# Optimization experiments

Hardware: AMD Instinct MI355X
Metric: run time of the kernel (lower is better)

Reference implementation:

```python
import jax, jax.numpy as jnp
import numpy as np

N_INTT = 100000
N_MVTX = 100000
N_EDGES = 300000
IN_DIM = 64
OUT_DIM = 64
FEAT_DIM = 2 * OUT_DIM          # 128
EDGE_DIM = 2 * FEAT_DIM         # 256
H_DIM = IN_DIM + FEAT_DIM + 2 * EDGE_DIM  # 64+128+512 = 704


def _lin(key, fan_in, fan_out):
    k1, k2 = jax.random.split(key)
    bound = 1.0 / np.sqrt(fan_in)
    W = jax.random.uniform(k1, (fan_in, fan_out), jnp.float32, -bound, bound)
    b = jax.random.uniform(k2, (fan_out,), jnp.float32, -bound, bound)
    return W, b


def setup_inputs() -> dict:
    key = jax.random.key(0)
    ks = jax.random.split(key, 12)
    x_intt_0 = jax.random.normal(ks[0], (N_INTT, 3), jnp.float32)
    x_mvtx_0 = jax.random.normal(ks[1], (N_MVTX, 3), jnp.float32)
    x_intt = jax.random.normal(ks[2], (N_INTT, IN_DIM), jnp.float32)
    x_mvtx = jax.random.normal(ks[3], (N_MVTX, IN_DIM), jnp.float32)
    start = jax.random.randint(ks[4], (N_EDGES,), 0, N_INTT, jnp.int32)
    end = jax.random.randint(ks[5], (N_EDGES,), 0, N_MVTX, jnp.int32)
    edge_index = jnp.stack([start, end], axis=0)
    W_in_intt, b_in_intt = _lin(ks[6], IN_DIM, FEAT_DIM)
    W_in_mvtx, b_in_mvtx = _lin(ks[7], IN_DIM, FEAT_DIM)
    W_score, b_score = _lin(ks[8], EDGE_DIM, 1)
    W_out_intt, b_out_intt = _lin(ks[9], H_DIM, OUT_DIM)
    W_out_mvtx, b_out_mvtx = _lin(ks[10], H_DIM, OUT_DIM)
    return {
        "x_intt_0": x_intt_0, "x_mvtx_0": x_mvtx_0,
        "x_intt": x_intt, "x_mvtx": x_mvtx, "edge_index": edge_index,
        "W_in_intt": W_in_intt, "b_in_intt": b_in_intt,
        "W_in_mvtx": W_in_mvtx, "b_in_mvtx": b_in_mvtx,
        "W_score": W_score, "b_score": b_score,
        "W_out_intt": W_out_intt, "b_out_intt": b_out_intt,
        "W_out_mvtx": W_out_mvtx, "b_out_mvtx": b_out_mvtx,
    }


def _mean_max_pool(edges, idx, num_segments):
    # scatter_mean with zero-initialized out: mean over incident edges, 0 if none
    s = jax.ops.segment_sum(edges, idx, num_segments=num_segments)
    cnt = jax.ops.segment_sum(jnp.ones((edges.shape[0], 1), edges.dtype), idx,
                              num_segments=num_segments)
    mean = s / jnp.maximum(cnt, 1.0)
    # scatter_max with zero-initialized out: max includes the initial 0
    mx = jnp.maximum(jax.ops.segment_max(edges, idx, num_segments=num_segments), 0.0)
    return mean, mx


def reference(x_intt_0, x_mvtx_0, x_intt, x_mvtx, edge_index,
              W_in_intt, b_in_intt, W_in_mvtx, b_in_mvtx,
              W_score, b_score, W_out_intt, b_out_intt,
              W_out_mvtx, b_out_mvtx):
    # apply_constraints=False -> x_intt_0/x_mvtx_0 unused
    xp_intt = x_intt @ W_in_intt + b_in_intt        # [Ni, F]
    xp_mvtx = x_mvtx @ W_in_mvtx + b_in_mvtx        # [Nm, F]
    start, end = edge_index[0], edge_index[1]
    xp = jnp.concatenate([xp_intt[start], xp_mvtx[end]], axis=-1)  # [E, 2F]
    att = jnp.exp(-jnp.abs(xp @ W_score + b_score))  # potential activation, [E,1]
    edges = xp * att                                 # [E, 2F]
    mean_i, max_i = _mean_max_pool(edges, start, xp_intt.shape[0])
    mean_m, max_m = _mean_max_pool(edges, end, xp_mvtx.shape[0])
    H_intt = jnp.concatenate([x_intt, xp_intt, mean_i, max_i], axis=-1)  # [Ni, 704]
    H_mvtx = jnp.concatenate([x_mvtx, xp_mvtx, mean_m, max_m], axis=-1)
    h_intt = jax.nn.relu(H_intt @ W_out_intt + b_out_intt)
    h_mvtx = jax.nn.relu(H_mvtx @ W_out_mvtx + b_out_mvtx)
    return (h_intt, h_mvtx)
```

## Files before the change

### kernel.cpp

```cpp
#include <hip/hip_runtime.h>
#include <hip/hip_bf16.h>

typedef __hip_bfloat16 bf16;
typedef __attribute__((ext_vector_type(8))) short bf16x8;
typedef __attribute__((ext_vector_type(4))) float f32x4;

__device__ __forceinline__ float bfu(unsigned u) { return __uint_as_float(u << 16); }
__device__ __forceinline__ unsigned packbf(float a, float b) {
    return (unsigned)__bfloat16_as_ushort(__float2bfloat16(a)) |
           ((unsigned)__bfloat16_as_ushort(__float2bfloat16(b)) << 16);
}

#define CAP 32

#define NEL_O (704 * 64)
#define NEL_I (64 * 128)
__global__ __launch_bounds__(256) void setup_kernel(
    const int* __restrict__ e_start, const int* __restrict__ e_end,
    int* __restrict__ deg_i, int* __restrict__ deg_m,
    int* __restrict__ list_i, int* __restrict__ list_m, int E, int fill_blocks,
    const float* __restrict__ Woi, const float* __restrict__ Wom,
    bf16* __restrict__ Wtoi, bf16* __restrict__ Wtom,
    const float* __restrict__ Wii, const float* __restrict__ Wim,
    bf16* __restrict__ Wtii, bf16* __restrict__ Wtim)
{
    if ((int)blockIdx.x < fill_blocks) {
        int i = blockIdx.x * 256 + threadIdx.x;
        if (i >= E) return;
        int s = e_start[i], e = e_end[i];
        int pi = atomicAdd(&deg_i[s], 1);
        if (pi < CAP) list_i[(size_t)s * CAP + pi] = e;
        int pm = atomicAdd(&deg_m[e], 1);
        if (pm < CAP) list_m[(size_t)e * CAP + pm] = s;
        return;
    }
    int tid = (blockIdx.x - fill_blocks) * 256 + threadIdx.x;
    if (tid < 2 * NEL_O) {
        int half = tid >= NEL_O;
        int t = tid - half * NEL_O;
        int j = t / 704, k = t % 704;
        const float* W = half ? Wom : Woi;
        bf16* Wt = half ? Wtom : Wtoi;
        Wt[(size_t)j * 704 + k] = __float2bfloat16(W[(size_t)k * 64 + j]);
        return;
    }
    int t2 = tid - 2 * NEL_O;
    if (t2 >= 2 * NEL_I) return;
    int half = t2 >= NEL_I;
    int t = t2 - half * NEL_I;
    int c = t / 64, k = t % 64;
    const float* W = half ? Wim : Wii;
    bf16* Wt = half ? Wtim : Wtii;
    Wt[(size_t)c * 64 + k] = __float2bfloat16(W[(size_t)k * 128 + c]);
}

__global__ __launch_bounds__(256) void lin_in_mfma(
    const float* __restrict__ x_i, const bf16* __restrict__ Wt_ii,
    const float* __restrict__ b_i,
    const float* __restrict__ x_m, const bf16* __restrict__ Wt_im,
    const float* __restrict__ b_m,
    const float* __restrict__ Wsc,
    bf16* __restrict__ xp_i, bf16* __restrict__ xp_m,
    float* __restrict__ sc_i, float* __restrict__ sc_m,
    int Ni, int Nm, int blocks_i)
{
    int side = (int)blockIdx.x >= blocks_i;
    int blk = side ? blockIdx.x - blocks_i : blockIdx.x;
    const float* x  = side ? x_m : x_i;
    const bf16* Wt  = side ? Wt_im : Wt_ii;
    const float* b  = side ? b_m : b_i;
    const float* wsc = side ? Wsc + 128 : Wsc;
    bf16* xp = side ? xp_m : xp_i;
    float* sc = side ? sc_m : sc_i;
    int N = side ? Nm : Ni;

    int tid = threadIdx.x, wv = tid >> 6, lane = tid & 63;
    int frow = lane & 15, kg = lane >> 4;
    int n0 = blk * 64 + wv * 16;
    if (n0 >= N) return;
    int nrow = min(n0 + frow, N - 1);
    f32x4 acc[8];
#pragma unroll
    for (int nt = 0; nt < 8; ++nt) acc[nt] = (f32x4){0.f, 0.f, 0.f, 0.f};
#pragma unroll
    for (int kk = 0; kk < 2; ++kk) {
        const float* ap = x + (size_t)nrow * 64 + kk * 32 + kg * 8;
        float4 a0 = *(const float4*)ap;
        float4 a1 = *(const float4*)(ap + 4);
        union { unsigned u[4]; bf16x8 v; } au;
        au.u[0] = packbf(a0.x, a0.y); au.u[1] = packbf(a0.z, a0.w);
        au.u[2] = packbf(a1.x, a1.y); au.u[3] = packbf(a1.z, a1.w);
#pragma unroll
        for (int nt = 0; nt < 8; ++nt) {
            bf16x8 bf = *(const bf16x8*)(Wt + (size_t)(nt * 16 + frow) * 64 + kk * 32 + kg * 8);
            acc[nt] = __builtin_amdgcn_mfma_f32_16x16x32_bf16(au.v, bf, acc[nt], 0, 0, 0);
        }
    }
    float contrib[4] = {0.f, 0.f, 0.f, 0.f};
#pragma unroll
    for (int nt = 0; nt < 8; ++nt) {
        int col = nt * 16 + frow;
        float bj = b[col];
        float wj = wsc[col];
#pragma unroll
        for (int reg = 0; reg < 4; ++reg) {
            float v = acc[nt][reg] + bj;
            int n = n0 + kg * 4 + reg;
            if (n < N) xp[(size_t)n * 128 + col] = __float2bfloat16(v);
            contrib[reg] += v * wj;
        }
    }
#pragma unroll
    for (int off = 1; off < 16; off <<= 1) {
#pragma unroll
        for (int reg = 0; reg < 4; ++reg)
            contrib[reg] += __shfl_xor(contrib[reg], off, 64);
    }
    if (frow == 0) {
#pragma unroll
        for (int reg = 0; reg < 4; ++reg) {
            int n = n0 + kg * 4 + reg;
            if (n < N) sc[n] = contrib[reg];
        }
    }
}

#define BN 16
#define HS 712
__device__ __forceinline__ void accum8(uint4 g, float att, float* s, float* m) {
    unsigned gg[4] = {g.x, g.y, g.z, g.w};
#pragma unroll
    for (int k = 0; k < 4; ++k) {
        float t0 = att * bfu(gg[k] & 0xffffu);
        float t1 = att * bfu(gg[k] >> 16);
        s[2 * k] += t0;  s[2 * k + 1] += t1;
        m[2 * k] = fmaxf(m[2 * k], t0);  m[2 * k + 1] = fmaxf(m[2 * k + 1], t1);
    }
}

__global__ __launch_bounds__(256) void node_kernel(
    const float* __restrict__ x_i, const bf16* __restrict__ xp_i,
    const bf16* __restrict__ xp_m,
    const float* __restrict__ sc_i, const float* __restrict__ sc_m,
    const int* __restrict__ deg_i, const int* __restrict__ list_i,
    const bf16* __restrict__ Wt_oi, const float* __restrict__ b_oi,
    const float* __restrict__ x_m,
    const int* __restrict__ deg_m, const int* __restrict__ list_m,
    const bf16* __restrict__ Wt_om, const float* __restrict__ b_om,
    const float* __restrict__ bsc, float* __restrict__ out,
    int Ni, int Nm, int blocks_i)
{
    __shared__ bf16 Hs[BN][HS];
    int side = (int)blockIdx.x >= blocks_i;
    int blk = side ? blockIdx.x - blocks_i : blockIdx.x;
    const float* x        = side ? x_m : x_i;
    const bf16* xp_self   = side ? xp_m : xp_i;
    const bf16* xp_other  = side ? xp_i : xp_m;
    const float* sc_self  = side ? sc_m : sc_i;
    const float* sc_other = side ? sc_i : sc_m;
    const int* deg  = side ? deg_m : deg_i;
    const int* list = side ? list_m : list_i;
    const bf16* Wt  = side ? Wt_om : Wt_oi;
    const float* b  = side ? b_om : b_oi;
    float* outp = side ? out + (size_t)Ni * 64 : out;
    int N = side ? Nm : Ni;
    int self_first = side ? 0 : 1;

    int tid = threadIdx.x, wv = tid >> 6, lane = tid & 63;
    int ql = lane & 15, q4 = lane & 48;
    int r = wv * 4 + (lane >> 4);
    int n0 = blk * BN;
    int n = min(n0 + r, N - 1);

    float bias = bsc[0];
    int dg = deg[n];
    int dgc = min(dg, CAP);
    float ps = sc_self[n] + bias;
    uint4 us4 = *(const uint4*)(xp_self + (size_t)n * 128 + ql * 8);
    float4 xv4 = *(const float4*)(x + (size_t)n * 64 + ql * 4);

    int oa = 0, ob = 0;
    float sa = 0.f, sb = 0.f;
    if (ql < dgc)      oa = list[(size_t)n * CAP + ql];
    if (16 + ql < dgc) ob = list[(size_t)n * CAP + 16 + ql];
    if (ql < dgc)      sa = sc_other[oa];
    if (16 + ql < dgc) sb = sc_other[ob];
    float att_a = (ql < dgc)      ? __expf(-fabsf(ps + sa)) : 0.f;
    float att_b = (16 + ql < dgc) ? __expf(-fabsf(ps + sb)) : 0.f;

    float A = att_a + att_b;
    float Am = fmaxf(att_a, att_b);
#pragma unroll
    for (int off = 1; off < 16; off <<= 1) {
        A += __shfl_xor(A, off, 64);
        Am = fmaxf(Am, __shfl_xor(Am, off, 64));
    }

    float s[8], m[8];
#pragma unroll
    for (int k = 0; k < 8; ++k) { s[k] = 0.f; m[k] = 0.f; }

    int dgm1 = max(dgc - 1, 0);
    uint4 g[8];
    float c[8];
#pragma unroll
    for (int d = 0; d < 8; ++d) {
        int dd = min(d, dgm1);
        int o = __shfl(oa, q4 + dd, 64);
        c[d] = (d < dgc) ? __shfl(att_a, q4 + dd, 64) : 0.f;
        g[d] = *(const uint4*)(xp_other + (size_t)o * 128 + ql * 8);
    }
#pragma unroll
    for (int d = 0; d < 8; ++d) accum8(g[d], c[d], s, m);

    for (int d = 8; d < dgc; d += 2) {
        int d1 = d + 1;
        int   o0 = (d  < 16) ? __shfl(oa, q4 + d, 64)     : __shfl(ob, q4 + d - 16, 64);
        float a0 = (d  < 16) ? __shfl(att_a, q4 + d, 64)  : __shfl(att_b, q4 + d - 16, 64);
        int   o1 = (d1 < 16) ? __shfl(oa, q4 + d1, 64)    : __shfl(ob, q4 + d1 - 16, 64);
        float a1 = (d1 < 16) ? __shfl(att_a, q4 + d1, 64) : __shfl(att_b, q4 + d1 - 16, 64);
        uint4 g0 = *(const uint4*)(xp_other + (size_t)o0 * 128 + ql * 8);
        uint4 g1 = *(const uint4*)(xp_other + (size_t)o1 * 128 + ql * 8);
        accum8(g0, a0, s, m);
        if (d1 < dgc) accum8(g1, a1, s, m);
    }

    float inv = 1.0f / fmaxf((float)dg, 1.0f);
    float sA = A * inv, sAm = Am;
    int cm_self  = self_first ? 192 : 320;
    int cm_cross = self_first ? 320 : 192;
    int cx_self  = self_first ? 448 : 576;
    int cx_cross = self_first ? 576 : 448;
    char* row = (char*)&Hs[r][0];
    *(uint2*)(row + ql * 8) = make_uint2(packbf(xv4.x, xv4.y), packbf(xv4.z, xv4.w));
    *(uint4*)(row + 128 + ql * 16) = us4;
    unsigned uu[4] = {us4.x, us4.y, us4.z, us4.w};
    float xs[8];
#pragma unroll
    for (int k = 0; k < 4; ++k) {
        xs[2 * k] = bfu(uu[k] & 0xffffu);
        xs[2 * k + 1] = bfu(uu[k] >> 16);
    }
    uint4 wms, wxs, wmc, wxc;
    wms.x = packbf(xs[0] * sA, xs[1] * sA);  wms.y = packbf(xs[2] * sA, xs[3] * sA);
    wms.z = packbf(xs[4] * sA, xs[5] * sA);  wms.w = packbf(xs[6] * sA, xs[7] * sA);
    wxs.x = packbf(fmaxf(xs[0], 0.f) * sAm, fmaxf(xs[1], 0.f) * sAm);
    wxs.y = packbf(fmaxf(xs[2], 0.f) * sAm, fmaxf(xs[3], 0.f) * sAm);
    wxs.z = packbf(fmaxf(xs[4], 0.f) * sAm, fmaxf(xs[5], 0.f) * sAm);
    wxs.w = packbf(fmaxf(xs[6], 0.f) * sAm, fmaxf(xs[7], 0.f) * sAm);
    wmc.x = packbf(s[0] * inv, s[1] * inv);  wmc.y = packbf(s[2] * inv, s[3] * inv);
    wmc.z = packbf(s[4] * inv, s[5] * inv);  wmc.w = packbf(s[6] * inv, s[7] * inv);
    wxc.x = packbf(m[0], m[1]);  wxc.y = packbf(m[2], m[3]);
    wxc.z = packbf(m[4], m[5]);  wxc.w = packbf(m[6], m[7]);
    *(uint4*)(row + cm_self * 2 + ql * 16)  = wms;
    *(uint4*)(row + cx_self * 2 + ql * 16)  = wxs;
    *(uint4*)(row + cm_cross * 2 + ql * 16) = wmc;
    *(uint4*)(row + cx_cross * 2 + ql * 16) = wxc;
    __syncthreads();

    int frow = lane & 15;
    int kg = lane >> 4;
    const char* abase = (const char*)&Hs[frow][0] + kg * 16;
    const char* bbase = (const char*)(Wt + (size_t)(wv * 16 + frow) * 704) + kg * 16;
    f32x4 acc = {0.f, 0.f, 0.f, 0.f};
#pragma unroll
    for (int kt = 0; kt < 22; ++kt) {
        bf16x8 a  = *(const bf16x8*)(abase + kt * 64);
        bf16x8 bf = *(const bf16x8*)(bbase + kt * 64);
        acc = __builtin_amdgcn_mfma_f32_16x16x32_bf16(a, bf, acc, 0, 0, 0);
    }
    int ccol = wv * 16 + frow;
    float bj = b[ccol];
#pragma unroll
    for (int reg = 0; reg < 4; ++reg) {
        int crow = kg * 4 + reg;
        int nn = n0 + crow;
        if (nn < N) outp[(size_t)nn * 64 + ccol] = fmaxf(acc[reg] + bj, 0.f);
    }
}

extern "C" void kernel_launch(void* const* d_in, const int* in_sizes, int n_in,
                              void* d_out, int out_size, void* d_ws, size_t ws_size,
                              hipStream_t stream) {
    const float* x_i    = (const float*)d_in[2];
    const float* x_m    = (const float*)d_in[3];
    const int*   eidx   = (const int*)d_in[4];
    const float* W_in_i = (const float*)d_in[5];
    const float* b_in_i = (const float*)d_in[6];
    const float* W_in_m = (const float*)d_in[7];
    const float* b_in_m = (const float*)d_in[8];
    const float* W_sc   = (const float*)d_in[9];
    const float* b_sc   = (const float*)d_in[10];
    const float* W_o_i  = (const float*)d_in[11];
    const float* b_o_i  = (const float*)d_in[12];
    const float* W_o_m  = (const float*)d_in[13];
    const float* b_o_m  = (const float*)d_in[14];

    int Ni = in_sizes[2] / 64;
    int Nm = in_sizes[3] / 64;
    int E  = in_sizes[4] / 2;
    const int* e_start = eidx;
    const int* e_end   = eidx + E;

    char* base = (char*)d_ws;
    bf16* xp_i  = (bf16*)base;  base += (size_t)Ni * 128 * sizeof(bf16);
    bf16* xp_m  = (bf16*)base;  base += (size_t)Nm * 128 * sizeof(bf16);
    float* sc_i = (float*)base; base += (size_t)Ni * sizeof(float);
    float* sc_m = (float*)base; base += (size_t)Nm * sizeof(float);
    int* list_i = (int*)base;   base += (size_t)Ni * CAP * sizeof(int);
    int* list_m = (int*)base;   base += (size_t)Nm * CAP * sizeof(int);
    int* deg_i  = (int*)base;   base += (size_t)Ni * sizeof(int);
    int* deg_m  = (int*)base;   base += (size_t)Nm * sizeof(int);
    bf16* Wt_oi = (bf16*)base;  base += (size_t)704 * 64 * sizeof(bf16);
    bf16* Wt_om = (bf16*)base;  base += (size_t)704 * 64 * sizeof(bf16);
    bf16* Wt_ii = (bf16*)base;  base += (size_t)128 * 64 * sizeof(bf16);
    bf16* Wt_im = (bf16*)base;  base += (size_t)128 * 64 * sizeof(bf16);
    hipMemsetAsync(deg_i, 0, ((size_t)Ni + Nm) * sizeof(int), stream);

    int fill_blocks = (E + 255) / 256;
    int wt_blocks = (2 * NEL_O + 2 * NEL_I + 255) / 256;
    setup_kernel<<<fill_blocks + wt_blocks, 256, 0, stream>>>(
        e_start, e_end, deg_i, deg_m, list_i, list_m, E, fill_blocks,
        W_o_i, W_o_m, Wt_oi, Wt_om, W_in_i, W_in_m, Wt_ii, Wt_im);

    int lin_bi = (Ni + 63) / 64, lin_bm = (Nm + 63) / 64;
    lin_in_mfma<<<lin_bi + lin_bm, 256, 0, stream>>>(
        x_i, Wt_ii, b_in_i, x_m, Wt_im, b_in_m, W_sc,
        xp_i, xp_m, sc_i, sc_m, Ni, Nm, lin_bi);

    float* out = (float*)d_out;
    int nb_i = (Ni + BN - 1) / BN, nb_m = (Nm + BN - 1) / BN;
    node_kernel<<<nb_i + nb_m, 256, 0, stream>>>(
        x_i, xp_i, xp_m, sc_i, sc_m, deg_i, list_i, Wt_oi, b_o_i,
        x_m, deg_m, list_m, Wt_om, b_o_m, b_sc, out, Ni, Nm, nb_i);
}
```

Measured before the change: 253.6 us.

## Fuse input linear into prep kernel and restructure neighbor gather loop

Merges the input-projection MFMA kernel into the setup kernel. The input weights are now read directly from fp32 with strided loads and converted to bf16 on the fly, so the separate transposed-weight buffer and one kernel launch go away. The neighbor gather loop now runs to the wave-wide maximum degree with clamped indices and zero weights, in pairs, replacing the prefetched 8-element batch plus tail loop. Risks are uncoalesced strided weight loads per MFMA tile and extra redundant gathers for low-degree nodes.

```diff
diff --git a/kernel.cpp b/kernel.cpp
--- a/kernel.cpp
+++ b/kernel.cpp
@@ -15,17 +15,25 @@
 
 #define NEL_O (704 * 64)
 #define NEL_I (64 * 128)
-__global__ __launch_bounds__(256) void setup_kernel(
+
+__global__ __launch_bounds__(256) void prep_kernel(
     const int* __restrict__ e_start, const int* __restrict__ e_end,
     int* __restrict__ deg_i, int* __restrict__ deg_m,
     int* __restrict__ list_i, int* __restrict__ list_m, int E, int fill_blocks,
     const float* __restrict__ Woi, const float* __restrict__ Wom,
     bf16* __restrict__ Wtoi, bf16* __restrict__ Wtom,
     const float* __restrict__ Wii, const float* __restrict__ Wim,
-    bf16* __restrict__ Wtii, bf16* __restrict__ Wtim)
+    bf16* __restrict__ Wtii, bf16* __restrict__ Wtim, int wt_blocks,
+    const float* __restrict__ x_i, const float* __restrict__ b_i,
+    const float* __restrict__ x_m, const float* __restrict__ b_m,
+    const float* __restrict__ Wsc,
+    bf16* __restrict__ xp_i, bf16* __restrict__ xp_m,
+    float* __restrict__ sc_i, float* __restrict__ sc_m,
+    int Ni, int Nm, int lin_bi)
 {
-    if ((int)blockIdx.x < fill_blocks) {
-        int i = blockIdx.x * 256 + threadIdx.x;
+    int bid = blockIdx.x;
+    if (bid < fill_blocks) {
+        int i = bid * 256 + threadIdx.x;
         if (i >= E) return;
         int s = e_start[i], e = e_end[i];
         int pi = atomicAdd(&deg_i[s], 1);
@@ -34,8 +42,10 @@
         if (pm < CAP) list_m[(size_t)e * CAP + pm] = s;
         return;
     }
-    int tid = (blockIdx.x - fill_blocks) * 256 + threadIdx.x;
-    if (tid < 2 * NEL_O) {
+    bid -= fill_blocks;
+    if (bid < wt_blocks) {
+        int tid = bid * 256 + threadIdx.x;
+        if (tid >= 2 * NEL_O) return;
         int half = tid >= NEL_O;
         int t = tid - half * NEL_O;
         int j = t / 704, k = t % 704;
@@ -44,31 +54,12 @@
         Wt[(size_t)j * 704 + k] = __float2bfloat16(W[(size_t)k * 64 + j]);
         return;
     }
-    int t2 = tid - 2 * NEL_O;
-    if (t2 >= 2 * NEL_I) return;
-    int half = t2 >= NEL_I;
-    int t = t2 - half * NEL_I;
-    int c = t / 64, k = t % 64;
-    const float* W = half ? Wim : Wii;
-    bf16* Wt = half ? Wtim : Wtii;
-    Wt[(size_t)c * 64 + k] = __float2bfloat16(W[(size_t)k * 128 + c]);
-}
-
-__global__ __launch_bounds__(256) void lin_in_mfma(
-    const float* __restrict__ x_i, const bf16* __restrict__ Wt_ii,
-    const float* __restrict__ b_i,
-    const float* __restrict__ x_m, const bf16* __restrict__ Wt_im,
-    const float* __restrict__ b_m,
-    const float* __restrict__ Wsc,
-    bf16* __restrict__ xp_i, bf16* __restrict__ xp_m,
-    float* __restrict__ sc_i, float* __restrict__ sc_m,
-    int Ni, int Nm, int blocks_i)
-{
-    int side = (int)blockIdx.x >= blocks_i;
-    int blk = side ? blockIdx.x - blocks_i : blockIdx.x;
-    const float* x  = side ? x_m : x_i;
-    const bf16* Wt  = side ? Wt_im : Wt_ii;
-    const float* b  = side ? b_m : b_i;
+    bid -= wt_blocks;
+    int side = bid >= lin_bi;
+    int blk = side ? bid - lin_bi : bid;
+    const float* x   = side ? x_m : x_i;
+    const float* Win = side ? Wim : Wii;
+    const float* b   = side ? b_m : b_i;
     const float* wsc = side ? Wsc + 128 : Wsc;
     bf16* xp = side ? xp_m : xp_i;
     float* sc = side ? sc_m : sc_i;
@@ -92,8 +83,13 @@
         au.u[2] = packbf(a1.x, a1.y); au.u[3] = packbf(a1.z, a1.w);
 #pragma unroll
         for (int nt = 0; nt < 8; ++nt) {
-            bf16x8 bf = *(const bf16x8*)(Wt + (size_t)(nt * 16 + frow) * 64 + kk * 32 + kg * 8);
-            acc[nt] = __builtin_amdgcn_mfma_f32_16x16x32_bf16(au.v, bf, acc[nt], 0, 0, 0);
+            int col = nt * 16 + frow;
+            const float* wp = Win + (size_t)(kk * 32 + kg * 8) * 128 + col;
+            union { unsigned u[4]; bf16x8 v; } bu;
+#pragma unroll
+            for (int z = 0; z < 4; ++z)
+                bu.u[z] = packbf(wp[(2 * z) * 128], wp[(2 * z + 1) * 128]);
+            acc[nt] = __builtin_amdgcn_mfma_f32_16x16x32_bf16(au.v, bu.v, acc[nt], 0, 0, 0);
         }
     }
     float contrib[4] = {0.f, 0.f, 0.f, 0.f};
@@ -200,29 +196,35 @@
 #pragma unroll
     for (int k = 0; k < 8; ++k) { s[k] = 0.f; m[k] = 0.f; }
 
+    int dmaxw = dgc;
+    dmaxw = max(dmaxw, __shfl_xor(dmaxw, 16, 64));
+    dmaxw = max(dmaxw, __shfl_xor(dmaxw, 32, 64));
     int dgm1 = max(dgc - 1, 0);
-    uint4 g[8];
-    float c[8];
-#pragma unroll
-    for (int d = 0; d < 8; ++d) {
-        int dd = min(d, dgm1);
-        int o = __shfl(oa, q4 + dd, 64);
-        c[d] = (d < dgc) ? __shfl(att_a, q4 + dd, 64) : 0.f;
-        g[d] = *(const uint4*)(xp_other + (size_t)o * 128 + ql * 8);
-    }
-#pragma unroll
-    for (int d = 0; d < 8; ++d) accum8(g[d], c[d], s, m);
-
-    for (int d = 8; d < dgc; d += 2) {
-        int d1 = d + 1;
-        int   o0 = (d  < 16) ? __shfl(oa, q4 + d, 64)     : __shfl(ob, q4 + d - 16, 64);
-        float a0 = (d  < 16) ? __shfl(att_a, q4 + d, 64)  : __shfl(att_b, q4 + d - 16, 64);
-        int   o1 = (d1 < 16) ? __shfl(oa, q4 + d1, 64)    : __shfl(ob, q4 + d1 - 16, 64);
-        float a1 = (d1 < 16) ? __shfl(att_a, q4 + d1, 64) : __shfl(att_b, q4 + d1 - 16, 64);
+
+    int dm0 = min(dmaxw, 16);
+    for (int d = 0; d < dm0; d += 2) {
+        int dc0 = min(d, dgm1), dc1 = min(d + 1, dgm1);
+        int   o0 = __shfl(oa, q4 + dc0, 64);
+        int   o1 = __shfl(oa, q4 + dc1, 64);
+        float a0 = (d < dgc)     ? __shfl(att_a, q4 + dc0, 64) : 0.f;
+        float a1 = (d + 1 < dgc) ? __shfl(att_a, q4 + dc1, 64) : 0.f;
         uint4 g0 = *(const uint4*)(xp_other + (size_t)o0 * 128 + ql * 8);
         uint4 g1 = *(const uint4*)(xp_other + (size_t)o1 * 128 + ql * 8);
         accum8(g0, a0, s, m);
-        if (d1 < dgc) accum8(g1, a1, s, m);
+        accum8(g1, a1, s, m);
+    }
+    for (int d = 16; d < dmaxw; d += 2) {
+        int dc0 = min(d, dgm1), dc1 = min(d + 1, dgm1);
+        int   o0 = (dc0 < 16) ? __shfl(oa, q4 + dc0, 64) : __shfl(ob, q4 + dc0 - 16, 64);
+        int   o1 = (dc1 < 16) ? __shfl(oa, q4 + dc1, 64) : __shfl(ob, q4 + dc1 - 16, 64);
+        float a0 = (d < dgc)     ? ((dc0 < 16) ? __shfl(att_a, q4 + dc0, 64)
+                                               : __shfl(att_b, q4 + dc0 - 16, 64)) : 0.f;
+        float a1 = (d + 1 < dgc) ? ((dc1 < 16) ? __shfl(att_a, q4 + dc1, 64)
+                                               : __shfl(att_b, q4 + dc1 - 16, 64)) : 0.f;
+        uint4 g0 = *(const uint4*)(xp_other + (size_t)o0 * 128 + ql * 8);
+        uint4 g1 = *(const uint4*)(xp_other + (size_t)o1 * 128 + ql * 8);
+        accum8(g0, a0, s, m);
+        accum8(g1, a1, s, m);
     }
 
     float inv = 1.0f / fmaxf((float)dg, 1.0f);
@@ -313,19 +315,15 @@
     int* deg_m  = (int*)base;   base += (size_t)Nm * sizeof(int);
     bf16* Wt_oi = (bf16*)base;  base += (size_t)704 * 64 * sizeof(bf16);
     bf16* Wt_om = (bf16*)base;  base += (size_t)704 * 64 * sizeof(bf16);
-    bf16* Wt_ii = (bf16*)base;  base += (size_t)128 * 64 * sizeof(bf16);
-    bf16* Wt_im = (bf16*)base;  base += (size_t)128 * 64 * sizeof(bf16);
     hipMemsetAsync(deg_i, 0, ((size_t)Ni + Nm) * sizeof(int), stream);
 
     int fill_blocks = (E + 255) / 256;
-    int wt_blocks = (2 * NEL_O + 2 * NEL_I + 255) / 256;
-    setup_kernel<<<fill_blocks + wt_blocks, 256, 0, stream>>>(
+    int wt_blocks = (2 * NEL_O + 255) / 256;
+    int lin_bi = (Ni + 63) / 64, lin_bm = (Nm + 63) / 64;
+    prep_kernel<<<fill_blocks + wt_blocks + lin_bi + lin_bm, 256, 0, stream>>>(
         e_start, e_end, deg_i, deg_m, list_i, list_m, E, fill_blocks,
-        W_o_i, W_o_m, Wt_oi, Wt_om, W_in_i, W_in_m, Wt_ii, Wt_im);
-
-    int lin_bi = (Ni + 63) / 64, lin_bm = (Nm + 63) / 64;
-    lin_in_mfma<<<lin_bi + lin_bm, 256, 0, stream>>>(
-        x_i, Wt_ii, b_in_i, x_m, Wt_im, b_in_m, W_sc,
+        W_o_i, W_o_m, Wt_oi, Wt_om, W_in_i, W_in_m, nullptr, nullptr, wt_blocks,
+        x_i, b_in_i, x_m, b_in_m, W_sc,
         xp_i, xp_m, sc_i, sc_m, Ni, Nm, lin_bi);
 
     float* out = (float*)d_out;
```

After: 219.1 us. -13.6%, faster.
